# Optimization experiments

Hardware: AMD Instinct MI355X
Metric: run time of the kernel (lower is better)

Reference implementation:

```python
import jax, jax.numpy as jnp
import numpy as np

D_MODEL = 1024
B, T = 4, 2048
LN_EPS = 1e-5


def setup_inputs() -> dict:
    key = jax.random.key(0)
    ks = jax.random.split(key, 8)
    d = D_MODEL
    x = jax.random.normal(ks[0], (B, T, d), dtype=jnp.float32)
    # linear params (fan-in scaled)
    W_in = jax.random.normal(ks[1], (d, 4 * d), dtype=jnp.float32) / np.sqrt(d)
    b_in = jnp.zeros((4 * d,), dtype=jnp.float32)
    W_out = jax.random.normal(ks[2], (2 * d, d), dtype=jnp.float32) / np.sqrt(2 * d)
    b_out = jnp.zeros((d,), dtype=jnp.float32)
    # LRU initializer (matches the torch module's initializer())
    rng = np.random.default_rng(0)
    r_min, r_max = 0.9, 0.999
    u1 = rng.random(d)
    u2 = rng.random(d)
    nu_log = np.log(-0.5 * np.log(u1 * (r_max ** 2 - r_min ** 2) + r_min ** 2))
    theta_log = np.log(u2 * np.pi * 2)
    gamma_log = np.log(np.sqrt(1 - np.exp(-np.exp(nu_log)) ** 2))
    # LayerNorm affine params
    ln_w = jnp.ones((2 * d,), dtype=jnp.float32)
    ln_b = jnp.zeros((2 * d,), dtype=jnp.float32)
    return {
        "x": x,
        "W_in": W_in, "b_in": b_in,
        "nu_log": jnp.asarray(nu_log, dtype=jnp.float32),
        "theta_log": jnp.asarray(theta_log, dtype=jnp.float32),
        "gamma_log": jnp.asarray(gamma_log, dtype=jnp.float32),
        "ln_w": ln_w, "ln_b": ln_b,
        "W_out": W_out, "b_out": b_out,
    }


def _complex_scan(in_r, in_i, f_r, f_i):
    """h_t = f * h_{t-1} + in_t over axis=1, complex math in real/imag pairs."""
    def combine(l, r):
        a1r, a1i, b1r, b1i = l
        a2r, a2i, b2r, b2i = r
        ar = a2r * a1r - a2i * a1i
        ai = a2r * a1i + a2i * a1r
        br = a2r * b1r - a2i * b1i + b2r
        bi = a2r * b1i + a2i * b1r + b2i
        return (ar, ai, br, bi)
    fr = jnp.broadcast_to(f_r, in_r.shape)
    fi = jnp.broadcast_to(f_i, in_i.shape)
    _, _, hr, hi = jax.lax.associative_scan(combine, (fr, fi, in_r, in_i), axis=1)
    return hr, hi


def reference(x, W_in, b_in, nu_log, theta_log, gamma_log, ln_w, ln_b, W_out, b_out):
    d = x.shape[-1]
    u = x @ W_in + b_in                       # [B, T, 4d]
    v, o = u[..., :2 * d], u[..., 2 * d:]     # each [B, T, 2d]
    nu = jnp.exp(-jnp.exp(nu_log))            # [d]
    theta = jnp.exp(theta_log)
    gamma = jnpp_exp = jnp.exp(gamma_log)
    f_r = nu * jnp.cos(theta)
    f_i = nu * jnp.sin(theta)
    in_r = gamma * v[..., :d]                 # [B, T, d]
    in_i = gamma * v[..., d:]
    h_r, h_i = _complex_scan(in_r, in_i, f_r, f_i)
    y = jnp.concatenate([h_r, h_i], axis=-1) * jax.nn.silu(o)  # [B, T, 2d]
    mu = jnp.mean(y, axis=-1, keepdims=True)
    var = jnp.mean(jnp.square(y - mu), axis=-1, keepdims=True)
    y = (y - mu) * jax.lax.rsqrt(var + LN_EPS) * ln_w + ln_b
    return y @ W_out + b_out                  # [B, T, d]
```

## Files before the change

kernel.cpp:

```cpp
#include <hip/hip_runtime.h>
#include <hip/hip_bf16.h>

#define D_MODEL 1024
#define BB 4
#define TT 2048
#define ROWS (BB*TT)
#define NCHUNK 32
#define CHLEN 64

typedef __attribute__((ext_vector_type(8))) short short8;
typedef __attribute__((ext_vector_type(4))) float floatx4;

static __device__ __forceinline__ ushort f2bf(float f) {
    union { float f; unsigned u; } v; v.f = f;
    unsigned r = v.u + 0x7FFF + ((v.u >> 16) & 1);
    return (ushort)(r >> 16);
}
static __device__ __forceinline__ float bf2f(ushort b) {
    union { unsigned u; float f; } v; v.u = ((unsigned)b) << 16;
    return v.f;
}

#define GLOAD_LDS16(gp, lp)                                                 \
    __builtin_amdgcn_global_load_lds(                                       \
        (const __attribute__((address_space(1))) void*)(gp),                \
        (__attribute__((address_space(3))) void*)(lp), 16, 0, 0)

#define PREP_A 8192
#define PREP_B 4096
#define PREP_C 2048
__global__ __launch_bounds__(256) void prep_all(
    const float* __restrict__ x, ushort* __restrict__ xb,
    const float* __restrict__ W_in, ushort* __restrict__ WinT,
    const float* __restrict__ W_out, ushort* __restrict__ W1T,
    const float* __restrict__ lnw, const float* __restrict__ lnb,
    float* __restrict__ s1, float* __restrict__ c2,
    const float* __restrict__ nu_log, const float* __restrict__ theta_log,
    const float* __restrict__ gamma_log,
    float* __restrict__ fr, float* __restrict__ fi, float* __restrict__ gm) {
    __shared__ float smem[32 * 33 + 8 * 32 * 2];
    int bid = blockIdx.x, tid = threadIdx.x;
    if (bid < PREP_A) {
        int i = bid * 256 + tid;
        float4 v = ((const float4*)x)[i];
        ushort4 o;
        o.x = f2bf(v.x); o.y = f2bf(v.y); o.z = f2bf(v.z); o.w = f2bf(v.w);
        ((ushort4*)xb)[i] = o;
    } else if (bid < PREP_A + PREP_B) {
        int b2 = bid - PREP_A;
        int n0 = (b2 & 127) * 32, k0 = (b2 >> 7) * 32;
        int tx = tid & 31, ty = tid >> 5;
        float (*tile)[33] = (float (*)[33])smem;
#pragma unroll
        for (int j = 0; j < 4; ++j)
            tile[ty + j*8][tx] = W_in[(size_t)(k0 + ty + j*8) * 4096 + n0 + tx];
        __syncthreads();
#pragma unroll
        for (int j = 0; j < 4; ++j)
            WinT[(size_t)(n0 + ty + j*8) * 1024 + k0 + tx] = f2bf(tile[tx][ty + j*8]);
    } else if (bid < PREP_A + PREP_B + PREP_C) {
        int b2 = bid - PREP_A - PREP_B;
        int n0 = (b2 & 31) * 32, k0 = (b2 >> 5) * 32;
        int tx = tid & 31, ty = tid >> 5;
        float (*tile)[33] = (float (*)[33])smem;
        float* red1 = smem + 32 * 33;
        float* red2 = red1 + 8 * 32;
        float p1 = 0.f, p2 = 0.f;
#pragma unroll
        for (int j = 0; j < 4; ++j) {
            int k = k0 + ty + j * 8;
            float w = W_out[(size_t)k * 1024 + n0 + tx];
            float lw = lnw[k], lb = lnb[k];
            tile[ty + j*8][tx] = lw * w;
            p1 += lw * w; p2 += lb * w;
        }
        __syncthreads();
#pragma unroll
        for (int j = 0; j < 4; ++j)
            W1T[(size_t)(n0 + ty + j*8) * 2048 + k0 + tx] = f2bf(tile[tx][ty + j*8]);
        red1[ty * 32 + tx] = p1; red2[ty * 32 + tx] = p2;
        __syncthreads();
        if (ty == 0) {
            float a = 0.f, b = 0.f;
#pragma unroll
            for (int t = 0; t < 8; ++t) { a += red1[t * 32 + tx]; b += red2[t * 32 + tx]; }
            atomicAdd(&s1[n0 + tx], a);
            atomicAdd(&c2[n0 + tx], b);
        }
    } else {
        int c = (bid - PREP_A - PREP_B - PREP_C) * 256 + tid;
        if (c < D_MODEL) {
            float nu = expf(-expf(nu_log[c]));
            float th = expf(theta_log[c]);
            fr[c] = nu * cosf(th);
            fi[c] = nu * sinf(th);
            gm[c] = expf(gamma_log[c]);
        }
    }
}

__global__ __launch_bounds__(256) void gemm_bf16(
    const ushort* __restrict__ A, const ushort* __restrict__ B,
    int K, int N, const float* __restrict__ bias, int mode,
    const float* __restrict__ gamma,
    ushort* __restrict__ out_r, ushort* __restrict__ out_i,
    ushort* __restrict__ out_o, float* __restrict__ outC,
    const float* __restrict__ mu, const float* __restrict__ rs,
    const float* __restrict__ s1, const float* __restrict__ c2) {
    __shared__ ushort As[128 * 64];
    __shared__ ushort Bs[128 * 64];
    int tid = threadIdx.x;
    int lane = tid & 63, wave = tid >> 6;
    int wm = (wave & 1) * 64, wn = (wave >> 1) * 64;
    int lr = lane & 15, q = lane >> 4;
    long m0 = (long)blockIdx.y * 128;
    long n0 = (long)blockIdx.x * 128;
    floatx4 acc[4][4] = {};

    int rs_ = tid >> 3;
    int pg = ((tid & 7) ^ (rs_ & 7)) * 8;
    const ushort* Ap = A + (m0 + rs_) * (long)K + pg;
    const ushort* Bp = B + (n0 + rs_) * (long)K + pg;
    int swl = lr & 7;

    for (int kt = 0; kt < K; kt += 64) {
        __syncthreads();
#pragma unroll
        for (int j = 0; j < 4; ++j) {
            GLOAD_LDS16(Ap + kt + (long)(j * 32) * K, &As[(j * 256 + tid) * 8]);
            GLOAD_LDS16(Bp + kt + (long)(j * 32) * K, &Bs[(j * 256 + tid) * 8]);
        }
        __syncthreads();
#pragma unroll
        for (int s = 0; s < 2; ++s) {
            short8 af[4], bfv[4];
            int pq = ((s * 4 + q) ^ swl) * 8;
#pragma unroll
            for (int r = 0; r < 4; ++r)
                af[r] = *(const short8*)&As[(wm + r * 16 + lr) * 64 + pq];
#pragma unroll
            for (int c = 0; c < 4; ++c)
                bfv[c] = *(const short8*)&Bs[(wn + c * 16 + lr) * 64 + pq];
#pragma unroll
            for (int r = 0; r < 4; ++r)
#pragma unroll
                for (int c = 0; c < 4; ++c)
                    acc[r][c] = __builtin_amdgcn_mfma_f32_16x16x32_bf16(
                        af[r], bfv[c], acc[r][c], 0, 0, 0);
        }
    }

    if (mode == 2) {
#pragma unroll
        for (int r = 0; r < 4; ++r) {
#pragma unroll
            for (int c = 0; c < 4; ++c) {
                long col = n0 + wn + c * 16 + lr;
                float bc = c2[col] + bias[col];
                float s1c = s1[col];
#pragma unroll
                for (int g = 0; g < 4; ++g) {
                    long row = m0 + wm + r * 16 + q * 4 + g;
                    outC[row * (long)N + col] =
                        rs[row] * (acc[r][c][g] - mu[row] * s1c) + bc;
                }
            }
        }
    } else {
        int sector = (int)((n0 + wn) >> 10);
        int lc0 = (int)((n0 + wn) & 1023);
        if (sector < 2) {
            ushort* dst = sector ? out_i : out_r;
#pragma unroll
            for (int r = 0; r < 4; ++r) {
#pragma unroll
                for (int c = 0; c < 4; ++c) {
                    int lc = lc0 + c * 16 + lr;
                    float bv = bias[(sector << 10) + lc];
                    float gv = gamma[lc];
#pragma unroll
                    for (int g = 0; g < 4; ++g) {
                        long row = m0 + wm + r * 16 + q * 4 + g;
                        dst[row * 1024 + lc] = f2bf(gv * (acc[r][c][g] + bv));
                    }
                }
            }
        } else {
            int oc0 = (int)(n0 + wn - 2048);
#pragma unroll
            for (int r = 0; r < 4; ++r) {
#pragma unroll
                for (int c = 0; c < 4; ++c) {
                    int oc = oc0 + c * 16 + lr;
                    float bv = bias[2048 + oc];
#pragma unroll
                    for (int g = 0; g < 4; ++g) {
                        long row = m0 + wm + r * 16 + q * 4 + g;
                        out_o[row * 2048 + oc] = f2bf(acc[r][c][g] + bv);
                    }
                }
            }
        }
    }
}

__global__ __launch_bounds__(256) void scan_carries(
    const ushort* __restrict__ in_r, const ushort* __restrict__ in_i,
    float* __restrict__ carry,
    const float* __restrict__ fr_, const float* __restrict__ fi_) {
    int t = blockIdx.x * 256 + threadIdx.x;
    int c = t & 1023;
    int ck = (t >> 10) & (NCHUNK - 1);
    int b = t >> 15;
    float fr = fr_[c], fi = fi_[c];
    size_t base = ((size_t)(b * TT + ck * CHLEN)) * 1024 + c;
    float hr = 0.f, hi = 0.f;
#pragma unroll 4
    for (int j = 0; j < CHLEN; ++j) {
        size_t idx = base + (size_t)j * 1024;
        float r = bf2f(in_r[idx]), im = bf2f(in_i[idx]);
        float nhr = fr * hr - fi * hi + r;
        float nhi = fr * hi + fi * hr + im;
        hr = nhr; hi = nhi;
    }
    size_t ci = (((size_t)b * 1024 + c) * NCHUNK + ck) * 2;
    carry[ci] = hr; carry[ci + 1] = hi;
}

__global__ __launch_bounds__(256) void scan_apply(
    const ushort* __restrict__ in_r, const ushort* __restrict__ in_i,
    const float* __restrict__ carry,
    const float* __restrict__ fr_, const float* __restrict__ fi_,
    const ushort* __restrict__ o, ushort* __restrict__ yb) {
    int t = blockIdx.x * 256 + threadIdx.x;
    int c = t & 1023;
    int ck = (t >> 10) & (NCHUNK - 1);
    int b = t >> 15;
    float fr = fr_[c], fi = fi_[c];
    float ar = fr, ai = fi;
#pragma unroll
    for (int s = 0; s < 6; ++s) {
        float nr = ar * ar - ai * ai, ni = 2.f * ar * ai;
        ar = nr; ai = ni;
    }
    float Hr = 0.f, Hi = 0.f;
    size_t cb = ((size_t)b * 1024 + c) * NCHUNK * 2;
    for (int k = 0; k < ck; ++k) {
        float cr = carry[cb + k * 2], cim = carry[cb + k * 2 + 1];
        float nHr = ar * Hr - ai * Hi + cr;
        float nHi = ar * Hi + ai * Hr + cim;
        Hr = nHr; Hi = nHi;
    }
    size_t base = ((size_t)(b * TT + ck * CHLEN)) * 1024 + c;
    size_t rowbase = (size_t)(b * TT + ck * CHLEN);
    float hr = Hr, hi = Hi;
#pragma unroll 2
    for (int j = 0; j < CHLEN; ++j) {
        size_t idx = base + (size_t)j * 1024;
        float r = bf2f(in_r[idx]), im = bf2f(in_i[idx]);
        float nhr = fr * hr - fi * hi + r;
        float nhi = fr * hi + fi * hr + im;
        hr = nhr; hi = nhi;
        size_t ob = (rowbase + j) * 2048 + c;
        float ov1 = bf2f(o[ob]);
        float ov2 = bf2f(o[ob + 1024]);
        float y1 = hr * ov1 / (1.f + __expf(-ov1));
        float y2 = hi * ov2 / (1.f + __expf(-ov2));
        yb[ob] = f2bf(y1);
        yb[ob + 1024] = f2bf(y2);
    }
}

__global__ __launch_bounds__(256) void row_stats(
    const ushort* __restrict__ yb, float* __restrict__ mu_o,
    float* __restrict__ rs_o) {
    long row = blockIdx.x;
    int tid = threadIdx.x;
    const ushort* p = yb + row * 2048 + tid * 8;
    uint4 raw = *(const uint4*)p;
    float s = 0.f, s2 = 0.f;
    unsigned w[4] = {raw.x, raw.y, raw.z, raw.w};
#pragma unroll
    for (int j = 0; j < 4; ++j) {
        float a = bf2f((ushort)(w[j] & 0xffff));
        float b = bf2f((ushort)(w[j] >> 16));
        s += a + b; s2 += a * a + b * b;
    }
#pragma unroll
    for (int off = 32; off > 0; off >>= 1) {
        s += __shfl_down(s, off, 64);
        s2 += __shfl_down(s2, off, 64);
    }
    __shared__ float red[8];
    int wv = tid >> 6;
    if ((tid & 63) == 0) { red[wv] = s; red[4 + wv] = s2; }
    __syncthreads();
    if (tid == 0) {
        s = red[0] + red[1] + red[2] + red[3];
        s2 = red[4] + red[5] + red[6] + red[7];
        float mu = s * (1.f / 2048.f);
        float var = s2 * (1.f / 2048.f) - mu * mu;
        mu_o[row] = mu;
        rs_o[row] = rsqrtf(var + 1e-5f);
    }
}


extern "C" void kernel_launch(void* const* d_in, const int* in_sizes, int n_in,
                              void* d_out, int out_size, void* d_ws, size_t ws_size,
                              hipStream_t stream) {
    const float* x         = (const float*)d_in[0];
    const float* W_in      = (const float*)d_in[1];
    const float* b_in      = (const float*)d_in[2];
    const float* nu_log    = (const float*)d_in[3];
    const float* theta_log = (const float*)d_in[4];
    const float* gamma_log = (const float*)d_in[5];
    const float* ln_w      = (const float*)d_in[6];
    const float* ln_b      = (const float*)d_in[7];
    const float* W_out     = (const float*)d_in[8];
    const float* b_out     = (const float*)d_in[9];
    float* out = (float*)d_out;

    char* ws = (char*)d_ws;
    size_t off = 0;
    auto alloc = [&](size_t bytes) {
        char* p = ws + off;
        off += (bytes + 255) & ~(size_t)255;
        return p;
    };
    ushort* xb    = (ushort*)alloc((size_t)ROWS * 1024 * 2);
    ushort* WinT  = (ushort*)alloc((size_t)4096 * 1024 * 2);
    ushort* W1T   = (ushort*)alloc((size_t)1024 * 2048 * 2);
    float*  fr    = (float*)alloc(1024 * 4);
    float*  fi    = (float*)alloc(1024 * 4);
    float*  gm    = (float*)alloc(1024 * 4);
    float*  s1c2  = (float*)alloc(2048 * 4);
    float*  s1    = s1c2;
    float*  c2    = s1c2 + 1024;
    ushort* in_r  = (ushort*)alloc((size_t)ROWS * 1024 * 2);
    ushort* in_i  = (ushort*)alloc((size_t)ROWS * 1024 * 2);
    ushort* obuf  = (ushort*)alloc((size_t)ROWS * 2048 * 2);
    float*  carry = (float*)alloc((size_t)BB * 1024 * NCHUNK * 2 * 4);
    ushort* yb    = (ushort*)alloc((size_t)ROWS * 2048 * 2);
    float*  muv   = (float*)alloc(ROWS * 4);
    float*  rsv   = (float*)alloc(ROWS * 4);

    hipMemsetAsync(s1c2, 0, 2048 * 4, stream);

    prep_all<<<PREP_A + PREP_B + PREP_C + 4, 256, 0, stream>>>(
        x, xb, W_in, WinT, W_out, W1T, ln_w, ln_b, s1, c2,
        nu_log, theta_log, gamma_log, fr, fi, gm);

    gemm_bf16<<<dim3(4096 / 128, ROWS / 128), 256, 0, stream>>>(
        xb, WinT, 1024, 4096, b_in, 1, gm, in_r, in_i, obuf, nullptr,
        nullptr, nullptr, nullptr, nullptr);

    scan_carries<<<BB * 1024 * NCHUNK / 256, 256, 0, stream>>>(in_r, in_i, carry, fr, fi);
    scan_apply<<<BB * 1024 * NCHUNK / 256, 256, 0, stream>>>(
        in_r, in_i, carry, fr, fi, obuf, yb);

    row_stats<<<ROWS, 256, 0, stream>>>(yb, muv, rsv);

    gemm_bf16<<<dim3(1024 / 128, ROWS / 128), 256, 0, stream>>>(
        yb, W1T, 2048, 1024, b_out, 2, nullptr, nullptr, nullptr, nullptr, out,
        muv, rsv, s1, c2);
}
```

Baseline: 295.4 us.

## Replace 128x128 GEMM with double-buffered 256x256 tile, 8-wave ping-pong kernel

Replaces the single-buffered 128x128 bf16 MFMA GEMM with a 256x256 tile kernel using 512 threads and double-buffered LDS. Global-to-LDS loads for upcoming k-tiles are interleaved between four MFMA quadrants, with barriers and s_setprio around the compute. This is meant to overlap memory with compute and raise data reuse per tile. In exchange it uses 128KB of LDS and more accumulator registers per thread. The second GEMM now launches only 128 blocks, which may underfill the GPU.

Result: slower. 315.2 us (+6.7%).

```diff
diff --git a/kernel.cpp b/kernel.cpp
--- a/kernel.cpp
+++ b/kernel.cpp
@@ -99,7 +99,15 @@
     }
 }
 
-__global__ __launch_bounds__(256) void gemm_bf16(
+#define P_PRE  do { __builtin_amdgcn_sched_barrier(0); __builtin_amdgcn_s_barrier();  \
+                    asm volatile("s_waitcnt lgkmcnt(0)" ::: "memory");                \
+                    __builtin_amdgcn_sched_barrier(0);                                \
+                    __builtin_amdgcn_s_setprio(1); } while (0)
+#define P_POST do { __builtin_amdgcn_s_setprio(0); __builtin_amdgcn_sched_barrier(0); \
+                    __builtin_amdgcn_s_barrier();                                     \
+                    __builtin_amdgcn_sched_barrier(0); } while (0)
+
+__global__ __launch_bounds__(512) void gemm256(
     const ushort* __restrict__ A, const ushort* __restrict__ B,
     int K, int N, const float* __restrict__ bias, int mode,
     const float* __restrict__ gamma,
@@ -107,101 +115,179 @@
     ushort* __restrict__ out_o, float* __restrict__ outC,
     const float* __restrict__ mu, const float* __restrict__ rs,
     const float* __restrict__ s1, const float* __restrict__ c2) {
-    __shared__ ushort As[128 * 64];
-    __shared__ ushort Bs[128 * 64];
+    __shared__ ushort LA[2][256 * 64];
+    __shared__ ushort LB[2][256 * 64];
     int tid = threadIdx.x;
-    int lane = tid & 63, wave = tid >> 6;
-    int wm = (wave & 1) * 64, wn = (wave >> 1) * 64;
+    int lane = tid & 63;
+    int wave = tid >> 6;
+    int wp = wave >> 2;
+    int wq = wave & 3;
     int lr = lane & 15, q = lane >> 4;
-    long m0 = (long)blockIdx.y * 128;
-    long n0 = (long)blockIdx.x * 128;
-    floatx4 acc[4][4] = {};
-
-    int rs_ = tid >> 3;
-    int pg = ((tid & 7) ^ (rs_ & 7)) * 8;
-    const ushort* Ap = A + (m0 + rs_) * (long)K + pg;
-    const ushort* Bp = B + (n0 + rs_) * (long)K + pg;
     int swl = lr & 7;
-
-    for (int kt = 0; kt < K; kt += 64) {
-        __syncthreads();
-#pragma unroll
-        for (int j = 0; j < 4; ++j) {
-            GLOAD_LDS16(Ap + kt + (long)(j * 32) * K, &As[(j * 256 + tid) * 8]);
-            GLOAD_LDS16(Bp + kt + (long)(j * 32) * K, &Bs[(j * 256 + tid) * 8]);
+    int rs8 = tid >> 3, ch = tid & 7;
+    int sw8 = (ch ^ (rs8 & 7)) * 8;
+    long m0 = (long)blockIdx.y * 256;
+    long n0 = (long)blockIdx.x * 256;
+    const int NT = K >> 6;
+
+    const ushort* Abase = A + (size_t)(m0 + rs8) * K + sw8;
+    const ushort* Bbase = B + (size_t)(n0 + rs8) * K + sw8;
+
+    floatx4 acc[8][4] = {};
+
+#define STG_A(kt, P, R) GLOAD_LDS16(Abase + (size_t)(R) * K + (kt), \
+                                    &LA[P][((R) + rs8) * 64 + ch * 8])
+#define STG_B(kt, P, R) GLOAD_LDS16(Bbase + (size_t)(R) * K + (kt), \
+                                    &LB[P][((R) + rs8) * 64 + ch * 8])
+
+    STG_A(0, 0, 0);    STG_A(0, 0, 64);
+    STG_B(0, 0, 0);    STG_B(0, 0, 64);
+    STG_B(0, 0, 128);  STG_B(0, 0, 192);
+    STG_A(0, 0, 128);  STG_A(0, 0, 192);
+    STG_A(64, 1, 0);   STG_A(64, 1, 64);
+    STG_B(64, 1, 0);   STG_B(64, 1, 64);
+    STG_B(64, 1, 128); STG_B(64, 1, 192);
+    asm volatile("s_waitcnt vmcnt(6)" ::: "memory");
+    __builtin_amdgcn_s_barrier();
+
+    for (int t = 0; t < NT; ++t) {
+        const int p = t & 1;
+        int kt1 = (t + 1 < NT) ? (t + 1) << 6 : 0;
+        int kt2 = (t + 2 < NT) ? (t + 2) << 6 : 0;
+        short8 a[2][4], b0[2][2], b1[2][2];
+
+#pragma unroll
+        for (int ks = 0; ks < 2; ++ks) {
+#pragma unroll
+            for (int r = 0; r < 4; ++r)
+                a[ks][r] = *(const short8*)&LA[p][(wp * 64 + r * 16 + lr) * 64 + ((ks * 4 + q) ^ swl) * 8];
+#pragma unroll
+            for (int c = 0; c < 2; ++c)
+                b0[ks][c] = *(const short8*)&LB[p][(wq * 32 + c * 16 + lr) * 64 + ((ks * 4 + q) ^ swl) * 8];
         }
-        __syncthreads();
-#pragma unroll
-        for (int s = 0; s < 2; ++s) {
-            short8 af[4], bfv[4];
-            int pq = ((s * 4 + q) ^ swl) * 8;
-#pragma unroll
-            for (int r = 0; r < 4; ++r)
-                af[r] = *(const short8*)&As[(wm + r * 16 + lr) * 64 + pq];
-#pragma unroll
-            for (int c = 0; c < 4; ++c)
-                bfv[c] = *(const short8*)&Bs[(wn + c * 16 + lr) * 64 + pq];
-#pragma unroll
-            for (int r = 0; r < 4; ++r)
-#pragma unroll
-                for (int c = 0; c < 4; ++c)
+        STG_A(kt1, p ^ 1, 128); STG_A(kt1, p ^ 1, 192);
+        P_PRE;
+#pragma unroll
+        for (int ks = 0; ks < 2; ++ks)
+#pragma unroll
+            for (int r = 0; r < 4; ++r)
+#pragma unroll
+                for (int c = 0; c < 2; ++c)
                     acc[r][c] = __builtin_amdgcn_mfma_f32_16x16x32_bf16(
-                        af[r], bfv[c], acc[r][c], 0, 0, 0);
-        }
-    }
+                        a[ks][r], b0[ks][c], acc[r][c], 0, 0, 0);
+        P_POST;
+
+#pragma unroll
+        for (int ks = 0; ks < 2; ++ks)
+#pragma unroll
+            for (int c = 0; c < 2; ++c)
+                b1[ks][c] = *(const short8*)&LB[p][(128 + wq * 32 + c * 16 + lr) * 64 + ((ks * 4 + q) ^ swl) * 8];
+        STG_A(kt2, p, 0); STG_A(kt2, p, 64);
+        P_PRE;
+#pragma unroll
+        for (int ks = 0; ks < 2; ++ks)
+#pragma unroll
+            for (int r = 0; r < 4; ++r)
+#pragma unroll
+                for (int c = 0; c < 2; ++c)
+                    acc[r][2 + c] = __builtin_amdgcn_mfma_f32_16x16x32_bf16(
+                        a[ks][r], b1[ks][c], acc[r][2 + c], 0, 0, 0);
+        P_POST;
+
+#pragma unroll
+        for (int ks = 0; ks < 2; ++ks)
+#pragma unroll
+            for (int r = 0; r < 4; ++r)
+                a[ks][r] = *(const short8*)&LA[p][(128 + wp * 64 + r * 16 + lr) * 64 + ((ks * 4 + q) ^ swl) * 8];
+        STG_B(kt2, p, 0); STG_B(kt2, p, 64);
+        P_PRE;
+#pragma unroll
+        for (int ks = 0; ks < 2; ++ks)
+#pragma unroll
+            for (int r = 0; r < 4; ++r)
+#pragma unroll
+                for (int c = 0; c < 2; ++c)
+                    acc[4 + r][c] = __builtin_amdgcn_mfma_f32_16x16x32_bf16(
+                        a[ks][r], b0[ks][c], acc[4 + r][c], 0, 0, 0);
+        P_POST;
+
+        STG_B(kt2, p, 128); STG_B(kt2, p, 192);
+        asm volatile("s_waitcnt vmcnt(6)" ::: "memory");
+        P_PRE;
+#pragma unroll
+        for (int ks = 0; ks < 2; ++ks)
+#pragma unroll
+            for (int r = 0; r < 4; ++r)
+#pragma unroll
+                for (int c = 0; c < 2; ++c)
+                    acc[4 + r][2 + c] = __builtin_amdgcn_mfma_f32_16x16x32_bf16(
+                        a[ks][r], b1[ks][c], acc[4 + r][2 + c], 0, 0, 0);
+        P_POST;
+    }
+    asm volatile("s_waitcnt vmcnt(0)" ::: "memory");
 
     if (mode == 2) {
 #pragma unroll
-        for (int r = 0; r < 4; ++r) {
-#pragma unroll
-            for (int c = 0; c < 4; ++c) {
-                long col = n0 + wn + c * 16 + lr;
+        for (int nh = 0; nh < 2; ++nh)
+#pragma unroll
+            for (int c = 0; c < 2; ++c) {
+                long col = n0 + nh * 128 + wq * 32 + c * 16 + lr;
                 float bc = c2[col] + bias[col];
                 float s1c = s1[col];
 #pragma unroll
-                for (int g = 0; g < 4; ++g) {
-                    long row = m0 + wm + r * 16 + q * 4 + g;
-                    outC[row * (long)N + col] =
-                        rs[row] * (acc[r][c][g] - mu[row] * s1c) + bc;
-                }
+                for (int mh = 0; mh < 2; ++mh)
+#pragma unroll
+                    for (int r = 0; r < 4; ++r)
+#pragma unroll
+                        for (int g = 0; g < 4; ++g) {
+                            long row = m0 + mh * 128 + wp * 64 + r * 16 + q * 4 + g;
+                            outC[row * (long)N + col] =
+                                rs[row] * (acc[mh * 4 + r][nh * 2 + c][g] - mu[row] * s1c) + bc;
+                        }
             }
-        }
     } else {
-        int sector = (int)((n0 + wn) >> 10);
-        int lc0 = (int)((n0 + wn) & 1023);
+        int sector = (int)(n0 >> 10);
         if (sector < 2) {
             ushort* dst = sector ? out_i : out_r;
 #pragma unroll
-            for (int r = 0; r < 4; ++r) {
-#pragma unroll
-                for (int c = 0; c < 4; ++c) {
-                    int lc = lc0 + c * 16 + lr;
+            for (int nh = 0; nh < 2; ++nh)
+#pragma unroll
+                for (int c = 0; c < 2; ++c) {
+                    int lc = (int)(n0 & 1023) + nh * 128 + wq * 32 + c * 16 + lr;
                     float bv = bias[(sector << 10) + lc];
                     float gv = gamma[lc];
 #pragma unroll
-                    for (int g = 0; g < 4; ++g) {
-                        long row = m0 + wm + r * 16 + q * 4 + g;
-                        dst[row * 1024 + lc] = f2bf(gv * (acc[r][c][g] + bv));
-                    }
+                    for (int mh = 0; mh < 2; ++mh)
+#pragma unroll
+                        for (int r = 0; r < 4; ++r)
+#pragma unroll
+                            for (int g = 0; g < 4; ++g) {
+                                long row = m0 + mh * 128 + wp * 64 + r * 16 + q * 4 + g;
+                                dst[row * 1024 + lc] = f2bf(gv * (acc[mh * 4 + r][nh * 2 + c][g] + bv));
+                            }
                 }
-            }
         } else {
-            int oc0 = (int)(n0 + wn - 2048);
-#pragma unroll
-            for (int r = 0; r < 4; ++r) {
-#pragma unroll
-                for (int c = 0; c < 4; ++c) {
-                    int oc = oc0 + c * 16 + lr;
+            int oc0 = (int)(n0 - 2048);
+#pragma unroll
+            for (int nh = 0; nh < 2; ++nh)
+#pragma unroll
+                for (int c = 0; c < 2; ++c) {
+                    int oc = oc0 + nh * 128 + wq * 32 + c * 16 + lr;
                     float bv = bias[2048 + oc];
 #pragma unroll
-                    for (int g = 0; g < 4; ++g) {
-                        long row = m0 + wm + r * 16 + q * 4 + g;
-                        out_o[row * 2048 + oc] = f2bf(acc[r][c][g] + bv);
-                    }
+                    for (int mh = 0; mh < 2; ++mh)
+#pragma unroll
+                        for (int r = 0; r < 4; ++r)
+#pragma unroll
+                            for (int g = 0; g < 4; ++g) {
+                                long row = m0 + mh * 128 + wp * 64 + r * 16 + q * 4 + g;
+                                out_o[row * 2048 + oc] = f2bf(acc[mh * 4 + r][nh * 2 + c][g] + bv);
+                            }
                 }
-            }
         }
     }
+#undef STG_A
+#undef STG_B
 }
 
 __global__ __launch_bounds__(256) void scan_carries(
@@ -351,7 +437,7 @@
         x, xb, W_in, WinT, W_out, W1T, ln_w, ln_b, s1, c2,
         nu_log, theta_log, gamma_log, fr, fi, gm);
 
-    gemm_bf16<<<dim3(4096 / 128, ROWS / 128), 256, 0, stream>>>(
+    gemm256<<<dim3(4096 / 256, ROWS / 256), 512, 0, stream>>>(
         xb, WinT, 1024, 4096, b_in, 1, gm, in_r, in_i, obuf, nullptr,
         nullptr, nullptr, nullptr, nullptr);
 
@@ -361,7 +447,7 @@
 
     row_stats<<<ROWS, 256, 0, stream>>>(yb, muv, rsv);
 
-    gemm_bf16<<<dim3(1024 / 128, ROWS / 128), 256, 0, stream>>>(
+    gemm256<<<dim3(1024 / 256, ROWS / 256), 512, 0, stream>>>(
         yb, W1T, 2048, 1024, b_out, 2, nullptr, nullptr, nullptr, nullptr, out,
         muv, rsv, s1, c2);
 }
```
